# Kernel tuning notes

Hardware: AMD Instinct MI355X
Metric: run time of the kernel (lower is better)

The kernel has to match this reference:

```python
import jax, jax.numpy as jnp
import numpy as np

HIDDEN = 512
IN_DIM = 512
N_ACT = 64
N_AGENTS = 8


def kalei_linear(x, ids, W, b, t):
    """x: [N, I]; ids: [N]; W: [O, I]; b: [O]; t: [A, O, I] -> [N, O].
    w_a = sign(W) * relu(|W| - sigmoid(t_a)); y_n = w_{ids[n]} @ x_n + b.
    """
    Wm = jnp.sign(W)[None] * jax.nn.relu(jnp.abs(W)[None] - jax.nn.sigmoid(t))  # [A,O,I]
    y = jnp.einsum('aoi,ni->nao', Wm, x)          # [N, A, O] batched masked GEMM
    y = jnp.take_along_axis(y, ids[:, None, None], axis=1)[:, 0]  # [N, O]
    return y + b[None, :]


def gru_cell(x, h, w_ih, w_hh, b_ih, b_hh):
    gi = x @ w_ih.T + b_ih
    gh = h @ w_hh.T + b_hh
    i_r, i_z, i_n = jnp.split(gi, 3, axis=-1)
    h_r, h_z, h_n = jnp.split(gh, 3, axis=-1)
    r = jax.nn.sigmoid(i_r + h_r)
    z = jax.nn.sigmoid(i_z + h_z)
    n = jnp.tanh(i_n + r * h_n)
    return (1.0 - z) * n + z * h


def setup_inputs() -> dict:
    key = jax.random.key(0)
    ks = jax.random.split(key, 20)
    B, A = 2048, N_AGENTS
    scale_init_lo, scale_init_hi = 3.0, 4.0  # -(rand*scale + bias) in [-4, -3]

    def thr(k, o, i):
        return -jax.random.uniform(k, (A, o, i), jnp.float32, scale_init_lo, scale_init_hi)

    w_scale = 0.05
    inp = {
        'inputs': jax.random.normal(ks[0], (B, A, IN_DIM), jnp.float32),
        'hidden_state': jax.random.normal(ks[1], (B, A, HIDDEN), jnp.float32),
        'agent_ids': jax.random.randint(ks[2], (B, A), 0, A),
        'fc1_w': jax.random.normal(ks[3], (HIDDEN, IN_DIM), jnp.float32) * w_scale,
        'fc1_b': jax.random.normal(ks[4], (HIDDEN,), jnp.float32) * w_scale,
        'fc1_t': thr(ks[5], HIDDEN, IN_DIM),
        'gru_wih': jax.random.normal(ks[6], (3 * HIDDEN, HIDDEN), jnp.float32) * w_scale,
        'gru_whh': jax.random.normal(ks[7], (3 * HIDDEN, HIDDEN), jnp.float32) * w_scale,
        'gru_bih': jax.random.normal(ks[8], (3 * HIDDEN,), jnp.float32) * w_scale,
        'gru_bhh': jax.random.normal(ks[9], (3 * HIDDEN,), jnp.float32) * w_scale,
        'fc2_w': jax.random.normal(ks[10], (HIDDEN, HIDDEN), jnp.float32) * w_scale,
        'fc2_b': jax.random.normal(ks[11], (HIDDEN,), jnp.float32) * w_scale,
        'fc2_t': thr(ks[12], HIDDEN, HIDDEN),
        'fc3_w': jax.random.normal(ks[13], (HIDDEN, HIDDEN), jnp.float32) * w_scale,
        'fc3_b': jax.random.normal(ks[14], (HIDDEN,), jnp.float32) * w_scale,
        'fc3_t': thr(ks[15], HIDDEN, HIDDEN),
        'fc4_w': jax.random.normal(ks[16], (N_ACT, HIDDEN), jnp.float32) * w_scale,
        'fc4_b': jax.random.normal(ks[17], (N_ACT,), jnp.float32) * w_scale,
        'fc4_t': thr(ks[18], N_ACT, HIDDEN),
    }
    return inp


def reference(inputs, hidden_state, agent_ids,
              fc1_w, fc1_b, fc1_t,
              gru_wih, gru_whh, gru_bih, gru_bhh,
              fc2_w, fc2_b, fc2_t,
              fc3_w, fc3_b, fc3_t,
              fc4_w, fc4_b, fc4_t):
    b, a, e = inputs.shape
    x = inputs.reshape(-1, e)                  # [N, e]
    ids = agent_ids.reshape(-1)                # [N]
    h_in = hidden_state.reshape(-1, HIDDEN)    # [N, H]

    x = jax.nn.relu(kalei_linear(x, ids, fc1_w, fc1_b, fc1_t))
    h = gru_cell(x, h_in, gru_wih, gru_whh, gru_bih, gru_bhh)
    q = jax.nn.relu(kalei_linear(h, ids, fc2_w, fc2_b, fc2_t))
    q = jax.nn.relu(kalei_linear(q, ids, fc3_w, fc3_b, fc3_t))
    q = kalei_linear(q, ids, fc4_w, fc4_b, fc4_t)
    return q.reshape(b, a, -1), h.reshape(b, a, -1)
```

## Files before the change

### kernel.cpp

```cpp
#include <hip/hip_runtime.h>
#include <hip/hip_bf16.h>
#include <stdint.h>

#define HID 512
#define NACT 64
#define NAG 8
#define NR 16384
#define BMT 128
#define MAXTILES 136

typedef __bf16 bf16_t;
typedef __bf16 bf16x4 __attribute__((ext_vector_type(4)));
typedef __bf16 bf16x8 __attribute__((ext_vector_type(8)));
typedef float  f32x16 __attribute__((ext_vector_type(16)));

#define MFMA32(a,b,c) __builtin_amdgcn_mfma_f32_32x32x16_bf16((a),(b),(c),0,0,0)

#define OFF_META 0
#define OFF_PERM 4096
#define OFF_WM1  (128*1024)
#define OFF_WM2  (OFF_WM1 + NAG*HID*HID*2)
#define OFF_WM3  (OFF_WM2 + NAG*HID*HID*2)
#define OFF_WM4  (OFF_WM3 + NAG*HID*HID*2)
#define OFF_WIH  (OFF_WM4 + NAG*NACT*HID*2)
#define OFF_WHH  (OFF_WIH + 3*HID*HID*2)
#define OFF_XS   (OFF_WHH + 3*HID*HID*2)
#define OFF_HS   (OFF_XS + (size_t)NR*HID*2)
#define OFF_B1   (OFF_HS + (size_t)NR*HID*2)

__device__ inline void load_lds16(const void* g, void* l) {
  __builtin_amdgcn_global_load_lds((__attribute__((address_space(1))) void*)g,
                                   (__attribute__((address_space(3))) void*)l,
                                   16, 0, 0);
}

template<int N> __device__ inline void wait_vmcnt() {
  asm volatile("s_waitcnt vmcnt(%0)" :: "n"(N) : "memory");
}
__device__ inline void wait_lgkm0() {
  asm volatile("s_waitcnt lgkmcnt(0)" ::: "memory");
}
#define BAR() __builtin_amdgcn_s_barrier()

__device__ inline bf16x8 lds_frag(const bf16_t* base, int r, int cb) {
  return *(const bf16x8*)((const char*)base + r*128 + ((cb*16) ^ ((r&7)<<4)));
}

__device__ inline void store8bf(void* dst, float4 a, float4 b) {
  union { bf16_t h[8]; uint4 u; } p;
  p.h[0]=(bf16_t)a.x; p.h[1]=(bf16_t)a.y; p.h[2]=(bf16_t)a.z; p.h[3]=(bf16_t)a.w;
  p.h[4]=(bf16_t)b.x; p.h[5]=(bf16_t)b.y; p.h[6]=(bf16_t)b.z; p.h[7]=(bf16_t)b.w;
  *(uint4*)dst = p.u;
}

__device__ inline float kmask(float w, float t) {
  float s = 1.f / (1.f + __expf(-t));
  float m = fabsf(w) - s;
  return m > 0.f ? copysignf(m, w) : 0.f;
}
__device__ inline float sigm(float x) { return 1.f / (1.f + __expf(-x)); }
__device__ inline float tanh_f(float x) {
  float e = __expf(2.f * fabsf(x));
  return copysignf(1.f - 2.f/(e + 1.f), x);
}

__global__ void k_prep(const float* __restrict__ f1w, const float* __restrict__ f1t,
                       const float* __restrict__ f2w, const float* __restrict__ f2t,
                       const float* __restrict__ f3w, const float* __restrict__ f3t,
                       const float* __restrict__ f4w, const float* __restrict__ f4t,
                       const float* __restrict__ gih, const float* __restrict__ ghh,
                       bf16_t* __restrict__ wm1, bf16_t* __restrict__ wm2,
                       bf16_t* __restrict__ wm3, bf16_t* __restrict__ wm4,
                       bf16_t* __restrict__ wihb, bf16_t* __restrict__ whhb,
                       int* __restrict__ meta)
{
  const int tid = threadIdx.x;
  if (blockIdx.x == 0 && tid < 32) meta[tid] = 0;
  long v = (long)blockIdx.x * 256 + tid;
  const long VR1 = 524288;
  if (v < 3*VR1) {
    int which = (int)(v / VR1);
    long e = (v - (long)which*VR1) * 4;
    const float* W = which==0 ? f1w : (which==1 ? f2w : f3w);
    const float* T = which==0 ? f1t : (which==1 ? f2t : f3t);
    bf16_t* O = which==0 ? wm1 : (which==1 ? wm2 : wm3);
    long oi = e & (long)(HID*HID - 1);
    float4 w = *(const float4*)(W + oi);
    float4 t = *(const float4*)(T + e);
    bf16x4 o;
    o[0]=(bf16_t)kmask(w.x,t.x); o[1]=(bf16_t)kmask(w.y,t.y);
    o[2]=(bf16_t)kmask(w.z,t.z); o[3]=(bf16_t)kmask(w.w,t.w);
    *(bf16x4*)(O + e) = o;
  } else if (v < 3*VR1 + 65536) {
    long e = (v - 3*VR1) * 4;
    long oi = e & (long)(NACT*HID - 1);
    float4 w = *(const float4*)(f4w + oi);
    float4 t = *(const float4*)(f4t + e);
    bf16x4 o;
    o[0]=(bf16_t)kmask(w.x,t.x); o[1]=(bf16_t)kmask(w.y,t.y);
    o[2]=(bf16_t)kmask(w.z,t.z); o[3]=(bf16_t)kmask(w.w,t.w);
    *(bf16x4*)(wm4 + e) = o;
  } else if (v < 3*VR1 + 65536 + 196608) {
    long e = (v - (3*VR1 + 65536)) * 4;
    float4 x = *(const float4*)(gih + e);
    bf16x4 o; o[0]=(bf16_t)x.x; o[1]=(bf16_t)x.y; o[2]=(bf16_t)x.z; o[3]=(bf16_t)x.w;
    *(bf16x4*)(wihb + e) = o;
  } else if (v < 3*VR1 + 65536 + 2*196608) {
    long e = (v - (3*VR1 + 65536 + 196608)) * 4;
    float4 x = *(const float4*)(ghh + e);
    bf16x4 o; o[0]=(bf16_t)x.x; o[1]=(bf16_t)x.y; o[2]=(bf16_t)x.z; o[3]=(bf16_t)x.w;
    *(bf16x4*)(whhb + e) = o;
  }
}

__global__ void k_count(const int* __restrict__ ids, int* __restrict__ meta) {
  int n = blockIdx.x*256 + threadIdx.x;
  atomicAdd(&meta[ids[n]], 1);
}

__global__ void k_td(int* __restrict__ meta) {
  int off = 0, nt = 0;
  for (int a = 0; a < NAG; ++a) {
    int c = meta[a];
    meta[8+a] = off;
    for (int t = 0; t*BMT < c; ++t) {
      meta[32 + nt]  = off + t*BMT;
      meta[192 + nt] = (c - t*BMT < BMT) ? (c - t*BMT) : BMT;
      meta[352 + nt] = a;
      ++nt;
    }
    off += c;
  }
  meta[16] = nt;
}

__global__ void k_scatter(const int* __restrict__ ids, int* __restrict__ meta,
                          int* __restrict__ perm) {
  int n = blockIdx.x*256 + threadIdx.x;
  int a = ids[n];
  int pos = atomicAdd(&meta[8+a], 1);
  perm[pos] = n;
}

__global__ void k_gather(const float* __restrict__ inputs, const float* __restrict__ hidden,
                         const int* __restrict__ perm,
                         bf16_t* __restrict__ xs, bf16_t* __restrict__ hs)
{
  int tid = threadIdx.x;
  int rb = blockIdx.x*4 + (tid>>6);
  int m = rb & (NR-1);
  int src = perm[m];
  const float* sp; bf16_t* op;
  if (rb < NR) { sp = inputs + (size_t)src*HID; op = xs + (size_t)m*HID; }
  else         { sp = hidden + (size_t)src*HID; op = hs + (size_t)m*HID; }
  int c = (tid&63)*8;
  float4 v0 = *(const float4*)(sp + c);
  float4 v1 = *(const float4*)(sp + c + 4);
  store8bf(op + c, v0, v1);
}

template<int BN, int OTOT, int OUTMODE>
__global__ __launch_bounds__(256, 2)
void k_fc(const bf16_t* __restrict__ a_bf, const bf16_t* __restrict__ wbase,
          const float* __restrict__ bias,
          bf16_t* __restrict__ out_bf, float* __restrict__ out_f32,
          const int* __restrict__ meta, const int* __restrict__ perm)
{
  constexpr int FN  = BN/64;
  constexpr int NLB = BN/32;
  constexpr int NLD = 4 + NLB;
  const int bx = blockIdx.x;
  if (bx >= meta[16]) return;
  const int m0 = meta[32+bx], rows = meta[192+bx], agent = meta[352+bx];
  const int o0 = blockIdx.y * BN;
  const bf16_t* W = wbase + (size_t)agent * OTOT * HID;

  __shared__ bf16_t lds[2][(BMT + BN)*64];

  const int tid = threadIdx.x, lane = tid & 63, wid = tid >> 6;
  const int wrow = wid & 1, wcol = wid >> 1;
  const int gsw = (lane&7) ^ ((lane>>3)&7);
  const int lr8 = lane >> 3;

  f32x16 zero;
  #pragma unroll
  for (int i = 0; i < 16; ++i) zero[i] = 0.f;
  f32x16 acc[2][FN];
  #pragma unroll
  for (int i = 0; i < 2; ++i)
    #pragma unroll
    for (int j = 0; j < FN; ++j) acc[i][j] = zero;

  auto stage_part = [&](int kp, int s, int lo, int hi) {
    if (kp >= 8) return;
    const int k0 = kp * 64;
    bf16_t* LA = &lds[s][0];
    bf16_t* LB = &lds[s][BMT*64];
    #pragma unroll
    for (int i = 0; i < NLD; ++i) {
      if (i < lo || i >= hi) continue;
      if (i < 4) {
        int c = wid*4 + i;
        int r = c*8 + lr8;
        int rl = r < rows ? r : rows-1;
        load_lds16(a_bf + (size_t)(m0+rl)*HID + k0 + gsw*8, (char*)LA + c*1024);
      } else {
        int c = wid*NLB + (i-4);
        int r = c*8 + lr8;
        load_lds16(W + (size_t)(o0+r)*HID + k0 + gsw*8, (char*)LB + c*1024);
      }
    }
  };

  stage_part(0, 0, 0, NLD);
  for (int t = 0; t < 8; ++t) {
    wait_vmcnt<0>(); BAR();
    const bf16_t* LA = &lds[t&1][0];
    const bf16_t* LB = &lds[t&1][BMT*64];
    #pragma unroll
    for (int kk = 0; kk < 4; ++kk) {
      const int cbb = kk*2 + (lane>>5);
      bf16x8 af[2], bf[FN];
      #pragma unroll
      for (int fm = 0; fm < 2; ++fm)
        af[fm] = lds_frag(LA, wrow*64 + fm*32 + (lane&31), cbb);
      #pragma unroll
      for (int fn = 0; fn < FN; ++fn)
        bf[fn] = lds_frag(LB, wcol*(BN/2) + fn*32 + (lane&31), cbb);
      stage_part(t+1, (t+1)&1, kk*NLD/4, (kk+1)*NLD/4);
      BAR();
      wait_lgkm0();
      __builtin_amdgcn_s_setprio(1);
      #pragma unroll
      for (int fn = 0; fn < FN; ++fn)
        #pragma unroll
        for (int fm = 0; fm < 2; ++fm)
          acc[fm][fn] = MFMA32(af[fm], bf[fn], acc[fm][fn]);
      __builtin_amdgcn_s_setprio(0);
      BAR();
    }
  }

  #pragma unroll
  for (int fn = 0; fn < FN; ++fn) {
    int col = o0 + wcol*(BN/2) + fn*32 + (lane&31);
    float bv = bias[col];
    #pragma unroll
    for (int fm = 0; fm < 2; ++fm) {
      #pragma unroll
      for (int g = 0; g < 16; ++g) {
        int rl = wrow*64 + fm*32 + 4*(lane>>5) + (g&3) + 8*(g>>2);
        if (rl < rows) {
          float y = acc[fm][fn][g] + bv;
          if constexpr (OUTMODE == 0) {
            y = fmaxf(y, 0.f);
            out_bf[(size_t)(m0+rl)*OTOT + col] = (bf16_t)y;
          } else {
            out_f32[(size_t)perm[m0+rl]*OTOT + col] = y;
          }
        }
      }
    }
  }
}

__global__ __launch_bounds__(256, 2)
void k_gru(const bf16_t* __restrict__ x1, const bf16_t* __restrict__ hs,
           const float* __restrict__ hidden,
           const bf16_t* __restrict__ wih, const bf16_t* __restrict__ whh,
           const float* __restrict__ bih, const float* __restrict__ bhh,
           bf16_t* __restrict__ hbuf, float* __restrict__ hout,
           const int* __restrict__ perm)
{
  const int m0 = blockIdx.x * BMT;
  const int j0 = blockIdx.y * 64;
  const int tid = threadIdx.x, lane = tid & 63, wid = tid >> 6;
  const int wrow = wid & 1, wcol = wid >> 1;
  const int gsw = (lane&7) ^ ((lane>>3)&7);
  const int lr8 = lane >> 3;

  __shared__ bf16_t lds[2][(BMT + 192)*64];

  f32x16 zero;
  #pragma unroll
  for (int i = 0; i < 16; ++i) zero[i] = 0.f;
  f32x16 ar[2], az[2], an[2], ah[2];
  ar[0]=ar[1]=az[0]=az[1]=an[0]=an[1]=ah[0]=ah[1]=zero;

  auto stage_part = [&](int kp, int s, int lo, int hi) {
    if (kp >= 16) return;
    const bf16_t* A  = (kp < 8) ? x1  : hs;
    const bf16_t* Wg = (kp < 8) ? wih : whh;
    const int k0 = (kp & 7) * 64;
    bf16_t* LA = &lds[s][0];
    bf16_t* LB = &lds[s][BMT*64];
    #pragma unroll
    for (int i = 0; i < 10; ++i) {
      if (i < lo || i >= hi) continue;
      if (i < 4) {
        int c = wid*4 + i;
        int r = c*8 + lr8;
        load_lds16(A + (size_t)(m0+r)*HID + k0 + gsw*8, (char*)LA + c*1024);
      } else {
        int c = wid*6 + (i-4);
        int r = c*8 + lr8;
        int wr = (r>>6)*HID + j0 + (r&63);
        load_lds16(Wg + (size_t)wr*HID + k0 + gsw*8, (char*)LB + c*1024);
      }
    }
  };

  auto step = [&](int t, f32x16 (&a3)[2]) {
    wait_vmcnt<0>(); BAR();
    const bf16_t* LA = &lds[t&1][0];
    const bf16_t* LB = &lds[t&1][BMT*64];
    #pragma unroll
    for (int kk = 0; kk < 4; ++kk) {
      const int cbb = kk*2 + (lane>>5);
      bf16x8 af0 = lds_frag(LA, wrow*64 +      (lane&31), cbb);
      bf16x8 af1 = lds_frag(LA, wrow*64 + 32 + (lane&31), cbb);
      const int rb = wcol*32 + (lane&31);
      bf16x8 b0 = lds_frag(LB,        rb, cbb);
      bf16x8 b1 = lds_frag(LB + 4096, rb, cbb);
      bf16x8 b2 = lds_frag(LB + 8192, rb, cbb);
      stage_part(t+1, (t+1)&1, kk*10/4, (kk+1)*10/4);
      BAR();
      wait_lgkm0();
      __builtin_amdgcn_s_setprio(1);
      ar[0] = MFMA32(af0, b0, ar[0]); ar[1] = MFMA32(af1, b0, ar[1]);
      az[0] = MFMA32(af0, b1, az[0]); az[1] = MFMA32(af1, b1, az[1]);
      a3[0] = MFMA32(af0, b2, a3[0]); a3[1] = MFMA32(af1, b2, a3[1]);
      __builtin_amdgcn_s_setprio(0);
      BAR();
    }
  };

  stage_part(0, 0, 0, 10);
  for (int t = 0; t < 8; ++t)  step(t, an);
  for (int t = 8; t < 16; ++t) step(t, ah);

  const int col = j0 + wcol*32 + (lane&31);
  const float b_r  = bih[col]        + bhh[col];
  const float b_z  = bih[512 + col]  + bhh[512 + col];
  const float b_in = bih[1024 + col];
  const float b_hn = bhh[1024 + col];
  #pragma unroll
  for (int fm = 0; fm < 2; ++fm) {
    #pragma unroll
    for (int g = 0; g < 16; ++g) {
      int rl = wrow*64 + fm*32 + 4*(lane>>5) + (g&3) + 8*(g>>2);
      int m = m0 + rl;
      int src = perm[m];
      float hp = hidden[(size_t)src*HID + col];
      float rg = sigm(ar[fm][g] + b_r);
      float zg = sigm(az[fm][g] + b_z);
      float ng = tanh_f(an[fm][g] + b_in + rg*(ah[fm][g] + b_hn));
      float h  = (1.f - zg)*ng + zg*hp;
      hbuf[(size_t)m*HID + col] = (bf16_t)h;
      hout[(size_t)src*HID + col] = h;
    }
  }
}

extern "C" void kernel_launch(void* const* d_in, const int* in_sizes, int n_in,
                              void* d_out, int out_size, void* d_ws, size_t ws_size,
                              hipStream_t stream) {
  const float* inputs  = (const float*)d_in[0];
  const float* hidden  = (const float*)d_in[1];
  const int*   ids     = (const int*)  d_in[2];
  const float* fc1_w   = (const float*)d_in[3];
  const float* fc1_b   = (const float*)d_in[4];
  const float* fc1_t   = (const float*)d_in[5];
  const float* gru_wih = (const float*)d_in[6];
  const float* gru_whh = (const float*)d_in[7];
  const float* gru_bih = (const float*)d_in[8];
  const float* gru_bhh = (const float*)d_in[9];
  const float* fc2_w   = (const float*)d_in[10];
  const float* fc2_b   = (const float*)d_in[11];
  const float* fc2_t   = (const float*)d_in[12];
  const float* fc3_w   = (const float*)d_in[13];
  const float* fc3_b   = (const float*)d_in[14];
  const float* fc3_t   = (const float*)d_in[15];
  const float* fc4_w   = (const float*)d_in[16];
  const float* fc4_b   = (const float*)d_in[17];
  const float* fc4_t   = (const float*)d_in[18];

  char* ws = (char*)d_ws;
  int*    meta = (int*)   (ws + OFF_META);
  int*    perm = (int*)   (ws + OFF_PERM);
  bf16_t* wm1  = (bf16_t*)(ws + OFF_WM1);
  bf16_t* wm2  = (bf16_t*)(ws + OFF_WM2);
  bf16_t* wm3  = (bf16_t*)(ws + OFF_WM3);
  bf16_t* wm4  = (bf16_t*)(ws + OFF_WM4);
  bf16_t* wihb = (bf16_t*)(ws + OFF_WIH);
  bf16_t* whhb = (bf16_t*)(ws + OFF_WHH);
  bf16_t* xs   = (bf16_t*)(ws + OFF_XS);
  bf16_t* hs   = (bf16_t*)(ws + OFF_HS);
  bf16_t* b1   = (bf16_t*)(ws + OFF_B1);

  float* q_out = (float*)d_out;
  float* h_out = q_out + (size_t)NR * NACT;

  k_prep<<<7936, 256, 0, stream>>>(fc1_w, fc1_t, fc2_w, fc2_t, fc3_w, fc3_t,
                                   fc4_w, fc4_t, gru_wih, gru_whh,
                                   wm1, wm2, wm3, wm4, wihb, whhb, meta);
  k_count<<<64, 256, 0, stream>>>(ids, meta);
  k_td<<<1, 1, 0, stream>>>(meta);
  k_scatter<<<64, 256, 0, stream>>>(ids, meta, perm);
  k_gather<<<8192, 256, 0, stream>>>(inputs, hidden, perm, xs, hs);

  k_fc<128, HID, 0><<<dim3(MAXTILES, 4), 256, 0, stream>>>(
      xs, wm1, fc1_b, b1, nullptr, meta, perm);
  k_gru<<<dim3(NR/BMT, 8), 256, 0, stream>>>(b1, hs, hidden, wihb, whhb,
                                             gru_bih, gru_bhh, xs, h_out, perm);
  k_fc<128, HID, 0><<<dim3(MAXTILES, 4), 256, 0, stream>>>(
      xs, wm2, fc2_b, b1, nullptr, meta, perm);
  k_fc<128, HID, 0><<<dim3(MAXTILES, 4), 256, 0, stream>>>(
      b1, wm3, fc3_b, hs, nullptr, meta, perm);
  k_fc<64, NACT, 1><<<dim3(MAXTILES, 1), 256, 0, stream>>>(
      hs, wm4, fc4_b, nullptr, q_out, meta, perm);
}
```

Before: 331.1 us.

## Use 256-row tiles with 512 threads and two-stage-ahead prefetch pipeline

Doubles the M tile to 256 rows per block with 8 waves for the masked FC layers and the GRU kernel, adding a second tile descriptor table in metadata. The staging is reworked so the next-next k-slab is issued after computing the current one, with partial vmcnt waits replacing the per-kk interleaved loads and extra barriers. The weight tile is reused across more rows. In exchange, the grid has fewer blocks (fewer waves in flight, possible tail imbalance with per-agent padding) and more LDS per block.

New measurement: 348.2 us. +5.1%, slower.

```diff
diff --git a/kernel.cpp b/kernel.cpp
--- a/kernel.cpp
+++ b/kernel.cpp
@@ -6,8 +6,8 @@
 #define NACT 64
 #define NAG 8
 #define NR 16384
-#define BMT 128
-#define MAXTILES 136
+#define MAXT1 136
+#define MAXT2 72
 
 typedef __bf16 bf16_t;
 typedef __bf16 bf16x4 __attribute__((ext_vector_type(4)));
@@ -33,7 +33,6 @@
                                    (__attribute__((address_space(3))) void*)l,
                                    16, 0, 0);
 }
-
 template<int N> __device__ inline void wait_vmcnt() {
   asm volatile("s_waitcnt vmcnt(%0)" :: "n"(N) : "memory");
 }
@@ -45,14 +44,12 @@
 __device__ inline bf16x8 lds_frag(const bf16_t* base, int r, int cb) {
   return *(const bf16x8*)((const char*)base + r*128 + ((cb*16) ^ ((r&7)<<4)));
 }
-
 __device__ inline void store8bf(void* dst, float4 a, float4 b) {
   union { bf16_t h[8]; uint4 u; } p;
   p.h[0]=(bf16_t)a.x; p.h[1]=(bf16_t)a.y; p.h[2]=(bf16_t)a.z; p.h[3]=(bf16_t)a.w;
   p.h[4]=(bf16_t)b.x; p.h[5]=(bf16_t)b.y; p.h[6]=(bf16_t)b.z; p.h[7]=(bf16_t)b.w;
   *(uint4*)dst = p.u;
 }
-
 __device__ inline float kmask(float w, float t) {
   float s = 1.f / (1.f + __expf(-t));
   float m = fabsf(w) - s;
@@ -119,19 +116,26 @@
 }
 
 __global__ void k_td(int* __restrict__ meta) {
-  int off = 0, nt = 0;
+  int off = 0, nt = 0, nt2 = 0;
   for (int a = 0; a < NAG; ++a) {
     int c = meta[a];
     meta[8+a] = off;
-    for (int t = 0; t*BMT < c; ++t) {
-      meta[32 + nt]  = off + t*BMT;
-      meta[192 + nt] = (c - t*BMT < BMT) ? (c - t*BMT) : BMT;
+    for (int t = 0; t*128 < c; ++t) {
+      meta[32 + nt]  = off + t*128;
+      meta[192 + nt] = (c - t*128 < 128) ? (c - t*128) : 128;
       meta[352 + nt] = a;
       ++nt;
     }
+    for (int t = 0; t*256 < c; ++t) {
+      meta[520 + nt2] = off + t*256;
+      meta[600 + nt2] = (c - t*256 < 256) ? (c - t*256) : 256;
+      meta[680 + nt2] = a;
+      ++nt2;
+    }
     off += c;
   }
   meta[16] = nt;
+  meta[17] = nt2;
 }
 
 __global__ void k_scatter(const int* __restrict__ ids, int* __restrict__ meta,
@@ -159,91 +163,87 @@
   store8bf(op + c, v0, v1);
 }
 
-template<int BN, int OTOT, int OUTMODE>
-__global__ __launch_bounds__(256, 2)
-void k_fc(const bf16_t* __restrict__ a_bf, const bf16_t* __restrict__ wbase,
-          const float* __restrict__ bias,
-          bf16_t* __restrict__ out_bf, float* __restrict__ out_f32,
-          const int* __restrict__ meta, const int* __restrict__ perm)
+__global__ __launch_bounds__(512, 1)
+void k_fc512(const bf16_t* __restrict__ a_bf, const bf16_t* __restrict__ wbase,
+             const float* __restrict__ bias, bf16_t* __restrict__ out_bf,
+             const int* __restrict__ meta)
 {
-  constexpr int FN  = BN/64;
-  constexpr int NLB = BN/32;
-  constexpr int NLD = 4 + NLB;
   const int bx = blockIdx.x;
-  if (bx >= meta[16]) return;
-  const int m0 = meta[32+bx], rows = meta[192+bx], agent = meta[352+bx];
-  const int o0 = blockIdx.y * BN;
-  const bf16_t* W = wbase + (size_t)agent * OTOT * HID;
-
-  __shared__ bf16_t lds[2][(BMT + BN)*64];
+  if (bx >= meta[17]) return;
+  const int m0 = meta[520+bx], rows = meta[600+bx], agent = meta[680+bx];
+  const int o0 = blockIdx.y * 128;
+  const bf16_t* W = wbase + (size_t)agent * HID * HID;
+
+  __shared__ bf16_t lds[2][(256+128)*64];
 
   const int tid = threadIdx.x, lane = tid & 63, wid = tid >> 6;
-  const int wrow = wid & 1, wcol = wid >> 1;
+  const int wrow = wid & 3, wcol = wid >> 2;
   const int gsw = (lane&7) ^ ((lane>>3)&7);
   const int lr8 = lane >> 3;
 
   f32x16 zero;
   #pragma unroll
   for (int i = 0; i < 16; ++i) zero[i] = 0.f;
-  f32x16 acc[2][FN];
-  #pragma unroll
-  for (int i = 0; i < 2; ++i)
-    #pragma unroll
-    for (int j = 0; j < FN; ++j) acc[i][j] = zero;
-
-  auto stage_part = [&](int kp, int s, int lo, int hi) {
+  f32x16 acc[2][2];
+  acc[0][0]=acc[0][1]=acc[1][0]=acc[1][1]=zero;
+
+  auto stage = [&](int kp, int s) {
     if (kp >= 8) return;
     const int k0 = kp * 64;
     bf16_t* LA = &lds[s][0];
-    bf16_t* LB = &lds[s][BMT*64];
-    #pragma unroll
-    for (int i = 0; i < NLD; ++i) {
-      if (i < lo || i >= hi) continue;
-      if (i < 4) {
-        int c = wid*4 + i;
-        int r = c*8 + lr8;
-        int rl = r < rows ? r : rows-1;
-        load_lds16(a_bf + (size_t)(m0+rl)*HID + k0 + gsw*8, (char*)LA + c*1024);
-      } else {
-        int c = wid*NLB + (i-4);
-        int r = c*8 + lr8;
-        load_lds16(W + (size_t)(o0+r)*HID + k0 + gsw*8, (char*)LB + c*1024);
-      }
+    bf16_t* LB = &lds[s][256*64];
+    #pragma unroll
+    for (int i = 0; i < 4; ++i) {
+      int c = wid*4 + i;
+      int r = c*8 + lr8;
+      int rl = r < rows ? r : rows-1;
+      load_lds16(a_bf + (size_t)(m0+rl)*HID + k0 + gsw*8, (char*)LA + c*1024);
+    }
+    #pragma unroll
+    for (int i = 0; i < 2; ++i) {
+      int c = wid*2 + i;
+      int r = c*8 + lr8;
+      load_lds16(W + (size_t)(o0+r)*HID + k0 + gsw*8, (char*)LB + c*1024);
     }
   };
 
-  stage_part(0, 0, 0, NLD);
-  for (int t = 0; t < 8; ++t) {
-    wait_vmcnt<0>(); BAR();
+  auto compute = [&](int t) {
     const bf16_t* LA = &lds[t&1][0];
-    const bf16_t* LB = &lds[t&1][BMT*64];
+    const bf16_t* LB = &lds[t&1][256*64];
     #pragma unroll
     for (int kk = 0; kk < 4; ++kk) {
       const int cbb = kk*2 + (lane>>5);
-      bf16x8 af[2], bf[FN];
+      bf16x8 af[2], bfv[2];
       #pragma unroll
       for (int fm = 0; fm < 2; ++fm)
         af[fm] = lds_frag(LA, wrow*64 + fm*32 + (lane&31), cbb);
       #pragma unroll
-      for (int fn = 0; fn < FN; ++fn)
-        bf[fn] = lds_frag(LB, wcol*(BN/2) + fn*32 + (lane&31), cbb);
-      stage_part(t+1, (t+1)&1, kk*NLD/4, (kk+1)*NLD/4);
-      BAR();
+      for (int fn = 0; fn < 2; ++fn)
+        bfv[fn] = lds_frag(LB, wcol*64 + fn*32 + (lane&31), cbb);
       wait_lgkm0();
       __builtin_amdgcn_s_setprio(1);
       #pragma unroll
-      for (int fn = 0; fn < FN; ++fn)
+      for (int fn = 0; fn < 2; ++fn)
         #pragma unroll
         for (int fm = 0; fm < 2; ++fm)
-          acc[fm][fn] = MFMA32(af[fm], bf[fn], acc[fm][fn]);
+          acc[fm][fn] = MFMA32(af[fm], bfv[fn], acc[fm][fn]);
       __builtin_amdgcn_s_setprio(0);
       BAR();
     }
-  }
+  };
+
+  stage(0, 0); stage(1, 1);
+  for (int t = 0; t < 7; ++t) {
+    wait_vmcnt<6>(); BAR();
+    compute(t);
+    stage(t + 2, t & 1);
+  }
+  wait_vmcnt<0>(); BAR();
+  compute(7);
 
   #pragma unroll
-  for (int fn = 0; fn < FN; ++fn) {
-    int col = o0 + wcol*(BN/2) + fn*32 + (lane&31);
+  for (int fn = 0; fn < 2; ++fn) {
+    int col = o0 + wcol*64 + fn*32 + (lane&31);
     float bv = bias[col];
     #pragma unroll
     for (int fm = 0; fm < 2; ++fm) {
@@ -251,20 +251,15 @@
       for (int g = 0; g < 16; ++g) {
         int rl = wrow*64 + fm*32 + 4*(lane>>5) + (g&3) + 8*(g>>2);
         if (rl < rows) {
-          float y = acc[fm][fn][g] + bv;
-          if constexpr (OUTMODE == 0) {
-            y = fmaxf(y, 0.f);
-            out_bf[(size_t)(m0+rl)*OTOT + col] = (bf16_t)y;
-          } else {
-            out_f32[(size_t)perm[m0+rl]*OTOT + col] = y;
-          }
+          float y = fmaxf(acc[fm][fn][g] + bv, 0.f);
+          out_bf[(size_t)(m0+rl)*HID + col] = (bf16_t)y;
         }
       }
     }
   }
 }
 
-__global__ __launch_bounds__(256, 2)
+__global__ __launch_bounds__(512, 1)
 void k_gru(const bf16_t* __restrict__ x1, const bf16_t* __restrict__ hs,
            const float* __restrict__ hidden,
            const bf16_t* __restrict__ wih, const bf16_t* __restrict__ whh,
@@ -272,14 +267,14 @@
            bf16_t* __restrict__ hbuf, float* __restrict__ hout,
            const int* __restrict__ perm)
 {
-  const int m0 = blockIdx.x * BMT;
+  const int m0 = blockIdx.x * 256;
   const int j0 = blockIdx.y * 64;
   const int tid = threadIdx.x, lane = tid & 63, wid = tid >> 6;
-  const int wrow = wid & 1, wcol = wid >> 1;
+  const int wrow = wid & 3, wcol = wid >> 2;
   const int gsw = (lane&7) ^ ((lane>>3)&7);
   const int lr8 = lane >> 3;
 
-  __shared__ bf16_t lds[2][(BMT + 192)*64];
+  __shared__ bf16_t lds[2][(256+192)*64];
 
   f32x16 zero;
   #pragma unroll
@@ -287,33 +282,31 @@
   f32x16 ar[2], az[2], an[2], ah[2];
   ar[0]=ar[1]=az[0]=az[1]=an[0]=an[1]=ah[0]=ah[1]=zero;
 
-  auto stage_part = [&](int kp, int s, int lo, int hi) {
+  auto stage = [&](int kp, int s) {
     if (kp >= 16) return;
     const bf16_t* A  = (kp < 8) ? x1  : hs;
     const bf16_t* Wg = (kp < 8) ? wih : whh;
     const int k0 = (kp & 7) * 64;
     bf16_t* LA = &lds[s][0];
-    bf16_t* LB = &lds[s][BMT*64];
-    #pragma unroll
-    for (int i = 0; i < 10; ++i) {
-      if (i < lo || i >= hi) continue;
-      if (i < 4) {
-        int c = wid*4 + i;
-        int r = c*8 + lr8;
-        load_lds16(A + (size_t)(m0+r)*HID + k0 + gsw*8, (char*)LA + c*1024);
-      } else {
-        int c = wid*6 + (i-4);
-        int r = c*8 + lr8;
-        int wr = (r>>6)*HID + j0 + (r&63);
-        load_lds16(Wg + (size_t)wr*HID + k0 + gsw*8, (char*)LB + c*1024);
-      }
+    bf16_t* LB = &lds[s][256*64];
+    #pragma unroll
+    for (int i = 0; i < 4; ++i) {
+      int c = wid*4 + i;
+      int r = c*8 + lr8;
+      load_lds16(A + (size_t)(m0+r)*HID + k0 + gsw*8, (char*)LA + c*1024);
+    }
+    #pragma unroll
+    for (int i = 0; i < 3; ++i) {
+      int c = wid*3 + i;
+      int r = c*8 + lr8;
+      int wr = (r>>6)*HID + j0 + (r&63);
+      load_lds16(Wg + (size_t)wr*HID + k0 + gsw*8, (char*)LB + c*1024);
     }
   };
 
-  auto step = [&](int t, f32x16 (&a3)[2]) {
-    wait_vmcnt<0>(); BAR();
+  auto body = [&](int t, f32x16 (&a3)[2]) {
     const bf16_t* LA = &lds[t&1][0];
-    const bf16_t* LB = &lds[t&1][BMT*64];
+    const bf16_t* LB = &lds[t&1][256*64];
     #pragma unroll
     for (int kk = 0; kk < 4; ++kk) {
       const int cbb = kk*2 + (lane>>5);
@@ -323,8 +316,6 @@
       bf16x8 b0 = lds_frag(LB,        rb, cbb);
       bf16x8 b1 = lds_frag(LB + 4096, rb, cbb);
       bf16x8 b2 = lds_frag(LB + 8192, rb, cbb);
-      stage_part(t+1, (t+1)&1, kk*10/4, (kk+1)*10/4);
-      BAR();
       wait_lgkm0();
       __builtin_amdgcn_s_setprio(1);
       ar[0] = MFMA32(af0, b0, ar[0]); ar[1] = MFMA32(af1, b0, ar[1]);
@@ -335,9 +326,19 @@
     }
   };
 
-  stage_part(0, 0, 0, 10);
-  for (int t = 0; t < 8; ++t)  step(t, an);
-  for (int t = 8; t < 16; ++t) step(t, ah);
+  stage(0, 0); stage(1, 1);
+  for (int t = 0; t < 8; ++t) {
+    wait_vmcnt<7>(); BAR();
+    body(t, an);
+    stage(t + 2, t & 1);
+  }
+  for (int t = 8; t < 15; ++t) {
+    wait_vmcnt<7>(); BAR();
+    body(t, ah);
+    stage(t + 2, t & 1);
+  }
+  wait_vmcnt<0>(); BAR();
+  body(15, ah);
 
   const int col = j0 + wcol*32 + (lane&31);
   const float b_r  = bih[col]        + bhh[col];
@@ -358,6 +359,91 @@
       float h  = (1.f - zg)*ng + zg*hp;
       hbuf[(size_t)m*HID + col] = (bf16_t)h;
       hout[(size_t)src*HID + col] = h;
+    }
+  }
+}
+
+__global__ __launch_bounds__(256, 2)
+void k_fc4(const bf16_t* __restrict__ a_bf, const bf16_t* __restrict__ wbase,
+           const float* __restrict__ bias, float* __restrict__ out_f32,
+           const int* __restrict__ meta, const int* __restrict__ perm)
+{
+  const int bx = blockIdx.x;
+  if (bx >= meta[16]) return;
+  const int m0 = meta[32+bx], rows = meta[192+bx], agent = meta[352+bx];
+  const bf16_t* W = wbase + (size_t)agent * NACT * HID;
+
+  __shared__ bf16_t lds[2][(128 + 64)*64];
+
+  const int tid = threadIdx.x, lane = tid & 63, wid = tid >> 6;
+  const int wrow = wid & 1, wcol = wid >> 1;
+  const int gsw = (lane&7) ^ ((lane>>3)&7);
+  const int lr8 = lane >> 3;
+
+  f32x16 zero;
+  #pragma unroll
+  for (int i = 0; i < 16; ++i) zero[i] = 0.f;
+  f32x16 acc[2];
+  acc[0]=acc[1]=zero;
+
+  auto stage = [&](int kp, int s) {
+    if (kp >= 8) return;
+    const int k0 = kp * 64;
+    bf16_t* LA = &lds[s][0];
+    bf16_t* LB = &lds[s][128*64];
+    #pragma unroll
+    for (int i = 0; i < 4; ++i) {
+      int c = wid*4 + i;
+      int r = c*8 + lr8;
+      int rl = r < rows ? r : rows-1;
+      load_lds16(a_bf + (size_t)(m0+rl)*HID + k0 + gsw*8, (char*)LA + c*1024);
+    }
+    #pragma unroll
+    for (int i = 0; i < 2; ++i) {
+      int c = wid*2 + i;
+      int r = c*8 + lr8;
+      load_lds16(W + (size_t)r*HID + k0 + gsw*8, (char*)LB + c*1024);
+    }
+  };
+
+  auto compute = [&](int t) {
+    const bf16_t* LA = &lds[t&1][0];
+    const bf16_t* LB = &lds[t&1][128*64];
+    #pragma unroll
+    for (int kk = 0; kk < 4; ++kk) {
+      const int cbb = kk*2 + (lane>>5);
+      bf16x8 af[2];
+      #pragma unroll
+      for (int fm = 0; fm < 2; ++fm)
+        af[fm] = lds_frag(LA, wrow*64 + fm*32 + (lane&31), cbb);
+      bf16x8 bv = lds_frag(LB, wcol*32 + (lane&31), cbb);
+      wait_lgkm0();
+      __builtin_amdgcn_s_setprio(1);
+      acc[0] = MFMA32(af[0], bv, acc[0]);
+      acc[1] = MFMA32(af[1], bv, acc[1]);
+      __builtin_amdgcn_s_setprio(0);
+      BAR();
+    }
+  };
+
+  stage(0, 0); stage(1, 1);
+  for (int t = 0; t < 7; ++t) {
+    wait_vmcnt<6>(); BAR();
+    compute(t);
+    stage(t + 2, t & 1);
+  }
+  wait_vmcnt<0>(); BAR();
+  compute(7);
+
+  int col = wcol*32 + (lane&31);
+  float bv = bias[col];
+  #pragma unroll
+  for (int fm = 0; fm < 2; ++fm) {
+    #pragma unroll
+    for (int g = 0; g < 16; ++g) {
+      int rl = wrow*64 + fm*32 + 4*(lane>>5) + (g&3) + 8*(g>>2);
+      if (rl < rows)
+        out_f32[(size_t)perm[m0+rl]*NACT + col] = acc[fm][g] + bv;
     }
   }
 }
@@ -409,14 +495,10 @@
   k_scatter<<<64, 256, 0, stream>>>(ids, meta, perm);
   k_gather<<<8192, 256, 0, stream>>>(inputs, hidden, perm, xs, hs);
 
-  k_fc<128, HID, 0><<<dim3(MAXTILES, 4), 256, 0, stream>>>(
-      xs, wm1, fc1_b, b1, nullptr, meta, perm);
-  k_gru<<<dim3(NR/BMT, 8), 256, 0, stream>>>(b1, hs, hidden, wihb, whhb,
+  k_fc512<<<dim3(MAXT2, 4), 512, 0, stream>>>(xs, wm1, fc1_b, b1, meta);
+  k_gru<<<dim3(NR/256, 8), 512, 0, stream>>>(b1, hs, hidden, wihb, whhb,
                                              gru_bih, gru_bhh, xs, h_out, perm);
-  k_fc<128, HID, 0><<<dim3(MAXTILES, 4), 256, 0, stream>>>(
-      xs, wm2, fc2_b, b1, nullptr, meta, perm);
-  k_fc<128, HID, 0><<<dim3(MAXTILES, 4), 256, 0, stream>>>(
-      b1, wm3, fc3_b, hs, nullptr, meta, perm);
-  k_fc<64, NACT, 1><<<dim3(MAXTILES, 1), 256, 0, stream>>>(
-      hs, wm4, fc4_b, nullptr, q_out, meta, perm);
-}
+  k_fc512<<<dim3(MAXT2, 4), 512, 0, stream>>>(xs, wm2, fc2_b, b1, meta);
+  k_fc512<<<dim3(MAXT2, 4), 512, 0, stream>>>(b1, wm3, fc3_b, hs, meta);
+  k_fc4<<<dim3(MAXT1, 1), 256, 0, stream>>>(hs, wm4, fc4_b, q_out, meta, perm);
+}
```

## Restructure GEMM pipelines to prefetch two K-tiles ahead with fewer barriers

Applied to the files above, without the earlier changes.

The k_fc and k_gru main loops now issue global-to-LDS loads for tile t+2 right after computing tile t. They wait with a partial vmcnt so one tile's loads stay in flight, instead of splitting loads across four sub-steps that each carried extra barriers and an lgkmcnt wait. LDS fragment reads are software-pipelined in registers (A/B sets), so the next k-slice's reads overlap the current MFMAs. This removes most per-k barriers and exposes more memory latency hiding, at the cost of more live registers, which could affect occupancy at launch_bounds(256,2).

Result: no change. 324.7 us (-2.0%).

```diff
diff --git a/kernel.cpp b/kernel.cpp
--- a/kernel.cpp
+++ b/kernel.cpp
@@ -6,8 +6,7 @@
 #define NACT 64
 #define NAG 8
 #define NR 16384
-#define BMT 128
-#define MAXTILES 136
+#define MAXT1 136
 
 typedef __bf16 bf16_t;
 typedef __bf16 bf16x4 __attribute__((ext_vector_type(4)));
@@ -33,26 +32,20 @@
                                    (__attribute__((address_space(3))) void*)l,
                                    16, 0, 0);
 }
-
 template<int N> __device__ inline void wait_vmcnt() {
   asm volatile("s_waitcnt vmcnt(%0)" :: "n"(N) : "memory");
 }
-__device__ inline void wait_lgkm0() {
-  asm volatile("s_waitcnt lgkmcnt(0)" ::: "memory");
-}
 #define BAR() __builtin_amdgcn_s_barrier()
 
 __device__ inline bf16x8 lds_frag(const bf16_t* base, int r, int cb) {
   return *(const bf16x8*)((const char*)base + r*128 + ((cb*16) ^ ((r&7)<<4)));
 }
-
 __device__ inline void store8bf(void* dst, float4 a, float4 b) {
   union { bf16_t h[8]; uint4 u; } p;
   p.h[0]=(bf16_t)a.x; p.h[1]=(bf16_t)a.y; p.h[2]=(bf16_t)a.z; p.h[3]=(bf16_t)a.w;
   p.h[4]=(bf16_t)b.x; p.h[5]=(bf16_t)b.y; p.h[6]=(bf16_t)b.z; p.h[7]=(bf16_t)b.w;
   *(uint4*)dst = p.u;
 }
-
 __device__ inline float kmask(float w, float t) {
   float s = 1.f / (1.f + __expf(-t));
   float m = fabsf(w) - s;
@@ -123,9 +116,9 @@
   for (int a = 0; a < NAG; ++a) {
     int c = meta[a];
     meta[8+a] = off;
-    for (int t = 0; t*BMT < c; ++t) {
-      meta[32 + nt]  = off + t*BMT;
-      meta[192 + nt] = (c - t*BMT < BMT) ? (c - t*BMT) : BMT;
+    for (int t = 0; t*128 < c; ++t) {
+      meta[32 + nt]  = off + t*128;
+      meta[192 + nt] = (c - t*128 < 128) ? (c - t*128) : 128;
       meta[352 + nt] = a;
       ++nt;
     }
@@ -175,7 +168,7 @@
   const int o0 = blockIdx.y * BN;
   const bf16_t* W = wbase + (size_t)agent * OTOT * HID;
 
-  __shared__ bf16_t lds[2][(BMT + BN)*64];
+  __shared__ bf16_t lds[2][(128 + BN)*64];
 
   const int tid = threadIdx.x, lane = tid & 63, wid = tid >> 6;
   const int wrow = wid & 1, wcol = wid >> 1;
@@ -191,55 +184,64 @@
     #pragma unroll
     for (int j = 0; j < FN; ++j) acc[i][j] = zero;
 
-  auto stage_part = [&](int kp, int s, int lo, int hi) {
+  auto stage = [&](int kp, int s) {
     if (kp >= 8) return;
     const int k0 = kp * 64;
     bf16_t* LA = &lds[s][0];
-    bf16_t* LB = &lds[s][BMT*64];
-    #pragma unroll
-    for (int i = 0; i < NLD; ++i) {
-      if (i < lo || i >= hi) continue;
-      if (i < 4) {
-        int c = wid*4 + i;
-        int r = c*8 + lr8;
-        int rl = r < rows ? r : rows-1;
-        load_lds16(a_bf + (size_t)(m0+rl)*HID + k0 + gsw*8, (char*)LA + c*1024);
-      } else {
-        int c = wid*NLB + (i-4);
-        int r = c*8 + lr8;
-        load_lds16(W + (size_t)(o0+r)*HID + k0 + gsw*8, (char*)LB + c*1024);
+    bf16_t* LB = &lds[s][128*64];
+    #pragma unroll
+    for (int i = 0; i < 4; ++i) {
+      int c = wid*4 + i;
+      int r = c*8 + lr8;
+      int rl = r < rows ? r : rows-1;
+      load_lds16(a_bf + (size_t)(m0+rl)*HID + k0 + gsw*8, (char*)LA + c*1024);
+    }
+    #pragma unroll
+    for (int i = 0; i < NLB; ++i) {
+      int c = wid*NLB + i;
+      int r = c*8 + lr8;
+      load_lds16(W + (size_t)(o0+r)*HID + k0 + gsw*8, (char*)LB + c*1024);
+    }
+  };
+
+  auto body = [&](int t) {
+    const bf16_t* LA = &lds[t&1][0];
+    const bf16_t* LB = &lds[t&1][128*64];
+    bf16x8 a0A,a1A,b0A,b1A, a0B,a1B,b0B,b1B;
+    auto rd = [&](int kk, bf16x8& a0, bf16x8& a1, bf16x8& b0, bf16x8& b1) {
+      const int cbb = kk*2 + (lane>>5);
+      a0 = lds_frag(LA, wrow*64 +      (lane&31), cbb);
+      a1 = lds_frag(LA, wrow*64 + 32 + (lane&31), cbb);
+      b0 = lds_frag(LB, wcol*(BN/2) +      (lane&31), cbb);
+      if constexpr (FN == 2)
+        b1 = lds_frag(LB, wcol*(BN/2) + 32 + (lane&31), cbb);
+    };
+    auto mm = [&](bf16x8& a0, bf16x8& a1, bf16x8& b0, bf16x8& b1) {
+      __builtin_amdgcn_s_setprio(1);
+      acc[0][0] = MFMA32(a0, b0, acc[0][0]);
+      acc[1][0] = MFMA32(a1, b0, acc[1][0]);
+      if constexpr (FN == 2) {
+        acc[0][1] = MFMA32(a0, b1, acc[0][1]);
+        acc[1][1] = MFMA32(a1, b1, acc[1][1]);
       }
-    }
+      __builtin_amdgcn_s_setprio(0);
+    };
+    rd(0, a0A,a1A,b0A,b1A);
+    rd(1, a0B,a1B,b0B,b1B);  mm(a0A,a1A,b0A,b1A);
+    rd(2, a0A,a1A,b0A,b1A);  mm(a0B,a1B,b0B,b1B);
+    rd(3, a0B,a1B,b0B,b1B);  mm(a0A,a1A,b0A,b1A);
+    mm(a0B,a1B,b0B,b1B);
   };
 
-  stage_part(0, 0, 0, NLD);
-  for (int t = 0; t < 8; ++t) {
-    wait_vmcnt<0>(); BAR();
-    const bf16_t* LA = &lds[t&1][0];
-    const bf16_t* LB = &lds[t&1][BMT*64];
-    #pragma unroll
-    for (int kk = 0; kk < 4; ++kk) {
-      const int cbb = kk*2 + (lane>>5);
-      bf16x8 af[2], bf[FN];
-      #pragma unroll
-      for (int fm = 0; fm < 2; ++fm)
-        af[fm] = lds_frag(LA, wrow*64 + fm*32 + (lane&31), cbb);
-      #pragma unroll
-      for (int fn = 0; fn < FN; ++fn)
-        bf[fn] = lds_frag(LB, wcol*(BN/2) + fn*32 + (lane&31), cbb);
-      stage_part(t+1, (t+1)&1, kk*NLD/4, (kk+1)*NLD/4);
-      BAR();
-      wait_lgkm0();
-      __builtin_amdgcn_s_setprio(1);
-      #pragma unroll
-      for (int fn = 0; fn < FN; ++fn)
-        #pragma unroll
-        for (int fm = 0; fm < 2; ++fm)
-          acc[fm][fn] = MFMA32(af[fm], bf[fn], acc[fm][fn]);
-      __builtin_amdgcn_s_setprio(0);
-      BAR();
-    }
-  }
+  stage(0, 0); stage(1, 1);
+  for (int t = 0; t < 7; ++t) {
+    wait_vmcnt<NLD>(); BAR();
+    body(t);
+    BAR();
+    stage(t + 2, t & 1);
+  }
+  wait_vmcnt<0>(); BAR();
+  body(7);
 
   #pragma unroll
   for (int fn = 0; fn < FN; ++fn) {
@@ -272,14 +274,14 @@
            bf16_t* __restrict__ hbuf, float* __restrict__ hout,
            const int* __restrict__ perm)
 {
-  const int m0 = blockIdx.x * BMT;
+  const int m0 = blockIdx.x * 128;
   const int j0 = blockIdx.y * 64;
   const int tid = threadIdx.x, lane = tid & 63, wid = tid >> 6;
   const int wrow = wid & 1, wcol = wid >> 1;
   const int gsw = (lane&7) ^ ((lane>>3)&7);
   const int lr8 = lane >> 3;
 
-  __shared__ bf16_t lds[2][(BMT + 192)*64];
+  __shared__ bf16_t lds[2][(128+192)*64];
 
   f32x16 zero;
   #pragma unroll
@@ -287,57 +289,70 @@
   f32x16 ar[2], az[2], an[2], ah[2];
   ar[0]=ar[1]=az[0]=az[1]=an[0]=an[1]=ah[0]=ah[1]=zero;
 
-  auto stage_part = [&](int kp, int s, int lo, int hi) {
+  auto stage = [&](int kp, int s) {
     if (kp >= 16) return;
     const bf16_t* A  = (kp < 8) ? x1  : hs;
     const bf16_t* Wg = (kp < 8) ? wih : whh;
     const int k0 = (kp & 7) * 64;
     bf16_t* LA = &lds[s][0];
-    bf16_t* LB = &lds[s][BMT*64];
-    #pragma unroll
-    for (int i = 0; i < 10; ++i) {
-      if (i < lo || i >= hi) continue;
-      if (i < 4) {
-        int c = wid*4 + i;
-        int r = c*8 + lr8;
-        load_lds16(A + (size_t)(m0+r)*HID + k0 + gsw*8, (char*)LA + c*1024);
-      } else {
-        int c = wid*6 + (i-4);
-        int r = c*8 + lr8;
-        int wr = (r>>6)*HID + j0 + (r&63);
-        load_lds16(Wg + (size_t)wr*HID + k0 + gsw*8, (char*)LB + c*1024);
-      }
+    bf16_t* LB = &lds[s][128*64];
+    #pragma unroll
+    for (int i = 0; i < 4; ++i) {
+      int c = wid*4 + i;
+      int r = c*8 + lr8;
+      load_lds16(A + (size_t)(m0+r)*HID + k0 + gsw*8, (char*)LA + c*1024);
+    }
+    #pragma unroll
+    for (int i = 0; i < 6; ++i) {
+      int c = wid*6 + i;
+      int r = c*8 + lr8;
+      int wr = (r>>6)*HID + j0 + (r&63);
+      load_lds16(Wg + (size_t)wr*HID + k0 + gsw*8, (char*)LB + c*1024);
     }
   };
 
-  auto step = [&](int t, f32x16 (&a3)[2]) {
-    wait_vmcnt<0>(); BAR();
+  auto body = [&](int t, f32x16 (&a3)[2]) {
     const bf16_t* LA = &lds[t&1][0];
-    const bf16_t* LB = &lds[t&1][BMT*64];
-    #pragma unroll
-    for (int kk = 0; kk < 4; ++kk) {
+    const bf16_t* LB = &lds[t&1][128*64];
+    bf16x8 a0A,a1A,b0A,b1A,b2A, a0B,a1B,b0B,b1B,b2B;
+    auto rd = [&](int kk, bf16x8& a0, bf16x8& a1, bf16x8& b0, bf16x8& b1, bf16x8& b2) {
       const int cbb = kk*2 + (lane>>5);
-      bf16x8 af0 = lds_frag(LA, wrow*64 +      (lane&31), cbb);
-      bf16x8 af1 = lds_frag(LA, wrow*64 + 32 + (lane&31), cbb);
+      a0 = lds_frag(LA, wrow*64 +      (lane&31), cbb);
+      a1 = lds_frag(LA, wrow*64 + 32 + (lane&31), cbb);
       const int rb = wcol*32 + (lane&31);
-      bf16x8 b0 = lds_frag(LB,        rb, cbb);
-      bf16x8 b1 = lds_frag(LB + 4096, rb, cbb);
-      bf16x8 b2 = lds_frag(LB + 8192, rb, cbb);
-      stage_part(t+1, (t+1)&1, kk*10/4, (kk+1)*10/4);
-      BAR();
-      wait_lgkm0();
+      b0 = lds_frag(LB,        rb, cbb);
+      b1 = lds_frag(LB + 4096, rb, cbb);
+      b2 = lds_frag(LB + 8192, rb, cbb);
+    };
+    auto mm = [&](bf16x8& a0, bf16x8& a1, bf16x8& b0, bf16x8& b1, bf16x8& b2) {
       __builtin_amdgcn_s_setprio(1);
-      ar[0] = MFMA32(af0, b0, ar[0]); ar[1] = MFMA32(af1, b0, ar[1]);
-      az[0] = MFMA32(af0, b1, az[0]); az[1] = MFMA32(af1, b1, az[1]);
-      a3[0] = MFMA32(af0, b2, a3[0]); a3[1] = MFMA32(af1, b2, a3[1]);
+      ar[0] = MFMA32(a0, b0, ar[0]); ar[1] = MFMA32(a1, b0, ar[1]);
+      az[0] = MFMA32(a0, b1, az[0]); az[1] = MFMA32(a1, b1, az[1]);
+      a3[0] = MFMA32(a0, b2, a3[0]); a3[1] = MFMA32(a1, b2, a3[1]);
       __builtin_amdgcn_s_setprio(0);
-      BAR();
-    }
+    };
+    rd(0, a0A,a1A,b0A,b1A,b2A);
+    rd(1, a0B,a1B,b0B,b1B,b2B);  mm(a0A,a1A,b0A,b1A,b2A);
+    rd(2, a0A,a1A,b0A,b1A,b2A);  mm(a0B,a1B,b0B,b1B,b2B);
+    rd(3, a0B,a1B,b0B,b1B,b2B);  mm(a0A,a1A,b0A,b1A,b2A);
+    mm(a0B,a1B,b0B,b1B,b2B);
   };
 
-  stage_part(0, 0, 0, 10);
-  for (int t = 0; t < 8; ++t)  step(t, an);
-  for (int t = 8; t < 16; ++t) step(t, ah);
+  stage(0, 0); stage(1, 1);
+  for (int t = 0; t < 8; ++t) {
+    wait_vmcnt<10>(); BAR();
+    body(t, an);
+    BAR();
+    stage(t + 2, t & 1);
+  }
+  for (int t = 8; t < 15; ++t) {
+    wait_vmcnt<10>(); BAR();
+    body(t, ah);
+    BAR();
+    stage(t + 2, t & 1);
+  }
+  wait_vmcnt<0>(); BAR();
+  body(15, ah);
 
   const int col = j0 + wcol*32 + (lane&31);
   const float b_r  = bih[col]        + bhh[col];
@@ -409,14 +424,14 @@
   k_scatter<<<64, 256, 0, stream>>>(ids, meta, perm);
   k_gather<<<8192, 256, 0, stream>>>(inputs, hidden, perm, xs, hs);
 
-  k_fc<128, HID, 0><<<dim3(MAXTILES, 4), 256, 0, stream>>>(
+  k_fc<128, HID, 0><<<dim3(MAXT1, 4), 256, 0, stream>>>(
       xs, wm1, fc1_b, b1, nullptr, meta, perm);
-  k_gru<<<dim3(NR/BMT, 8), 256, 0, stream>>>(b1, hs, hidden, wihb, whhb,
+  k_gru<<<dim3(NR/128, 8), 256, 0, stream>>>(b1, hs, hidden, wihb, whhb,
                                              gru_bih, gru_bhh, xs, h_out, perm);
-  k_fc<128, HID, 0><<<dim3(MAXTILES, 4), 256, 0, stream>>>(
+  k_fc<128, HID, 0><<<dim3(MAXT1, 4), 256, 0, stream>>>(
       xs, wm2, fc2_b, b1, nullptr, meta, perm);
-  k_fc<128, HID, 0><<<dim3(MAXTILES, 4), 256, 0, stream>>>(
+  k_fc<128, HID, 0><<<dim3(MAXT1, 4), 256, 0, stream>>>(
       b1, wm3, fc3_b, hs, nullptr, meta, perm);
-  k_fc<64, NACT, 1><<<dim3(MAXTILES, 1), 256, 0, stream>>>(
+  k_fc<64, NACT, 1><<<dim3(MAXT1, 1), 256, 0, stream>>>(
       hs, wm4, fc4_b, nullptr, q_out, meta, perm);
 }
```
